# Optimization experiments

Hardware: AMD Instinct MI355X
Metric: run time of the kernel (lower is better)

Reference implementation:

```python
import jax, jax.numpy as jnp
import numpy as np

MIDC = 128
HEADS = 8
HEADC = MIDC // HEADS
EPS = 1e-5


def setup_inputs() -> dict:
    key = jax.random.key(0)
    ks = jax.random.split(key, 8)
    B, C, H, W = 8, MIDC, 256, 256
    s = 1.0 / np.sqrt(C)
    x = jax.random.normal(ks[0], (B, C, H, W), dtype=jnp.float32)
    qkv_w = jax.random.normal(ks[1], (3 * C, C), dtype=jnp.float32) * s
    o1_w = jax.random.normal(ks[2], (C, C), dtype=jnp.float32) * s
    o2_w = jax.random.normal(ks[3], (C, C), dtype=jnp.float32) * s
    kln_w = 1.0 + 0.1 * jax.random.normal(ks[4], (HEADS, 1, HEADC), dtype=jnp.float32)
    kln_b = 0.1 * jax.random.normal(ks[5], (HEADS, 1, HEADC), dtype=jnp.float32)
    vln_w = 1.0 + 0.1 * jax.random.normal(ks[6], (HEADS, 1, HEADC), dtype=jnp.float32)
    vln_b = 0.1 * jax.random.normal(ks[7], (HEADS, 1, HEADC), dtype=jnp.float32)
    return {"x": x, "qkv_w": qkv_w, "o1_w": o1_w, "o2_w": o2_w,
            "kln_w": kln_w, "kln_b": kln_b, "vln_w": vln_w, "vln_b": vln_b}


def _ln(t, w, b):
    # torch LayerNorm variant: unbiased std, eps added to std (not variance)
    m = t.mean(-1, keepdims=True)
    s = jnp.std(t, axis=-1, ddof=1, keepdims=True)
    return w * ((t - m) / (s + EPS)) + b


def reference(x, qkv_w, o1_w, o2_w, kln_w, kln_b, vln_w, vln_b):
    B, C, H, W = x.shape
    hc = C // HEADS
    N = H * W
    # 1x1 conv == pointwise matmul over channel dim
    qkv = jnp.einsum('oc,bchw->bhwo', qkv_w, x)            # (B,H,W,3C)
    qkv = qkv.reshape(B, N, HEADS, 3 * hc).transpose(0, 2, 1, 3)  # (B,heads,N,3hc)
    q, k, v = jnp.split(qkv, 3, axis=-1)
    k = _ln(k, kln_w, kln_b)
    v = _ln(v, vln_w, vln_b)
    kv = jnp.einsum('bhnd,bhne->bhde', k, v) / N            # (B,heads,hc,hc)
    o = jnp.einsum('bhnd,bhde->bhne', q, kv)                # (B,heads,N,hc)
    o = o.transpose(0, 2, 1, 3).reshape(B, H, W, C).transpose(0, 3, 1, 2)
    ret = o + x
    u = jnp.einsum('oc,bchw->bohw', o1_w, ret)
    u = jax.nn.gelu(u, approximate=False)
    u = jnp.einsum('oc,bchw->bohw', o2_w, u) + x
    return jax.nn.gelu(u, approximate=False)
```

## Files before the change

### kernel.cpp

```cpp
#include <hip/hip_runtime.h>

#define EPS 1e-5f

typedef _Float16 half8_t __attribute__((ext_vector_type(8)));
typedef _Float16 half4_t __attribute__((ext_vector_type(4)));
typedef float    float4_t __attribute__((ext_vector_type(4)));

__device__ __forceinline__ float gelu_f(float v) {
  return 0.5f * v * (1.0f + erff(v * 0.70710678118654752f));
}

template<int CTRL>
__device__ __forceinline__ float dpp_add(float v) {
  int j = __builtin_amdgcn_update_dpp(0, __float_as_int(v), CTRL, 0xF, 0xF, true);
  return v + __int_as_float(j);
}
__device__ __forceinline__ float rsum16(float v) {
  v = dpp_add<0xB1>(v);
  v = dpp_add<0x4E>(v);
  v = dpp_add<0x124>(v);
  v = dpp_add<0x128>(v);
  return v;
}

__global__ __launch_bounds__(256)
void k_wconv(const float* __restrict__ qkvw, const float* __restrict__ o1w,
             const float* __restrict__ o2w, _Float16* __restrict__ kvw,
             _Float16* __restrict__ qw, _Float16* __restrict__ o1h,
             _Float16* __restrict__ o2h) {
  int t = blockIdx.x * 256 + threadIdx.x;
  if (t < 32768) {
    int r = t >> 7, c = t & 127;
    int src = (r >> 5) * 48 + 16 + (r & 31);
    kvw[t] = (_Float16)qkvw[src * 128 + c];
  } else if (t < 49152) {
    int i = t - 32768;
    int r = i >> 7, c = i & 127;
    int src = (r >> 4) * 48 + (r & 15);
    qw[i] = (_Float16)qkvw[src * 128 + c];
  } else if (t < 65536) {
    int i = t - 49152;
    o1h[i] = (_Float16)o1w[i];
  } else {
    int i = t - 65536;
    o2h[i] = (_Float16)o2w[i];
  }
}

__global__ __launch_bounds__(256, 3)
void k_qkv_kv(const float* __restrict__ x, const _Float16* __restrict__ kvw,
              const float* __restrict__ klw, const float* __restrict__ klb,
              const float* __restrict__ vlw, const float* __restrict__ vlb,
              float* __restrict__ partial) {
  __shared__ _Float16 xs[64][136];
  const int t = threadIdx.x;
  const int lane = t & 63, w = t >> 6;
  const int quad = lane >> 4, l16 = lane & 15;
  const int b = blockIdx.x >> 8, cb = blockIdx.x & 255;
  const float* xb = x + (long)b * 8388608;

  float kw0[2], kb0[2], vw0[2], vb0[2];
#pragma unroll
  for (int hh = 0; hh < 2; hh++) {
    int h = 2 * w + hh;
    kw0[hh] = klw[h * 16 + l16]; kb0[hh] = klb[h * 16 + l16];
    vw0[hh] = vlw[h * 16 + l16]; vb0[hh] = vlb[h * 16 + l16];
  }

  float4_t kvacc[2] = {};

  for (int ch = 0; ch < 4; ch++) {
    const int n0 = cb * 256 + ch * 64;
#pragma unroll
    for (int i = 0; i < 8; i++) {
      int f = i * 256 + t;
      int c = f >> 4, pg = f & 15;
      float4 v = *(const float4*)(xb + ((long)c << 16) + n0 + 4 * pg);
      xs[4 * pg + 0][c] = (_Float16)v.x;
      xs[4 * pg + 1][c] = (_Float16)v.y;
      xs[4 * pg + 2][c] = (_Float16)v.z;
      xs[4 * pg + 3][c] = (_Float16)v.w;
    }
    __syncthreads();

    float4_t acc[4][4] = {};
#pragma unroll
    for (int k = 0; k < 4; k++) {
      half8_t A[4];
#pragma unroll
      for (int mt = 0; mt < 4; mt++)
        A[mt] = *(const half8_t*)&xs[mt * 16 + l16][k * 32 + quad * 8];
#pragma unroll
      for (int ot = 0; ot < 4; ot++) {
        half8_t Bf = *(const half8_t*)(kvw + (w * 64 + ot * 16 + l16) * 128 + k * 32 + quad * 8);
#pragma unroll
        for (int mt = 0; mt < 4; mt++)
          acc[mt][ot] = __builtin_amdgcn_mfma_f32_16x16x32_f16(A[mt], Bf, acc[mt][ot], 0, 0, 0);
      }
    }

#pragma unroll
    for (int hh = 0; hh < 2; hh++) {
#pragma unroll
      for (int mt = 0; mt < 4; mt++) {
        half4_t kf, vf;
#pragma unroll
        for (int rr = 0; rr < 4; rr++) {
          float kx = acc[mt][2 * hh + 0][rr];
          float vx = acc[mt][2 * hh + 1][rr];
          float s1k = rsum16(kx), s2k = rsum16(kx * kx);
          float s1v = rsum16(vx), s2v = rsum16(vx * vx);
          float mk = s1k * 0.0625f;
          float vark = (s2k - s1k * mk) * (1.0f / 15.0f);
          float kn = kw0[hh] * (kx - mk) / (sqrtf(fmaxf(vark, 0.0f)) + EPS) + kb0[hh];
          float mv = s1v * 0.0625f;
          float varv = (s2v - s1v * mv) * (1.0f / 15.0f);
          float vn = vw0[hh] * (vx - mv) / (sqrtf(fmaxf(varv, 0.0f)) + EPS) + vb0[hh];
          kf[rr] = (_Float16)kn;
          vf[rr] = (_Float16)vn;
        }
        kvacc[hh] = __builtin_amdgcn_mfma_f32_16x16x16f16(kf, vf, kvacc[hh], 0, 0, 0);
      }
    }
    __syncthreads();
  }

#pragma unroll
  for (int hh = 0; hh < 2; hh++) {
    int h = 2 * w + hh;
#pragma unroll
    for (int rr = 0; rr < 4; rr++) {
      int d = quad * 4 + rr;
      partial[((long)blockIdx.x * 8 + h) * 256 + d * 16 + l16] = kvacc[hh][rr];
    }
  }
}

__global__ __launch_bounds__(256)
void k_reduce(const float* __restrict__ partial, float* __restrict__ kvT) {
  const int bh = blockIdx.x;
  const int t = threadIdx.x;
  const int b = bh >> 3, h = bh & 7;
  float s = 0.0f;
#pragma unroll 8
  for (int cb = 0; cb < 256; cb++)
    s += partial[((long)(b * 256 + cb) * 8 + h) * 256 + t];
  kvT[(bh << 8) + (t & 15) * 16 + (t >> 4)] = s * (1.0f / 65536.0f);
}

__device__ __forceinline__ void gemm_128(const _Float16* src, const _Float16* wgt,
                                         int w, int l16, int quad, float4_t (&acc)[4][2]) {
#pragma unroll
  for (int k = 0; k < 4; k++) {
    half8_t A[4];
#pragma unroll
    for (int mt = 0; mt < 4; mt++)
      A[mt] = *(const half8_t*)(src + (mt * 16 + l16) * 136 + k * 32 + quad * 8);
#pragma unroll
    for (int ot = 0; ot < 2; ot++) {
      half8_t Bf = *(const half8_t*)(wgt + (w * 32 + ot * 16 + l16) * 128 + k * 32 + quad * 8);
#pragma unroll
      for (int mt = 0; mt < 4; mt++)
        acc[mt][ot] = __builtin_amdgcn_mfma_f32_16x16x32_f16(A[mt], Bf, acc[mt][ot], 0, 0, 0);
    }
  }
}

__global__ __launch_bounds__(256, 3)
void k_attn_out(const float* __restrict__ x, const _Float16* __restrict__ qw,
                const _Float16* __restrict__ o1h, const _Float16* __restrict__ o2h,
                const float* __restrict__ kvT, float* __restrict__ out) {
  __shared__ _Float16 xs[64][136];
  __shared__ _Float16 us[64][136];
  __shared__ _Float16 rs[64][136];
  const int t = threadIdx.x;
  const int lane = t & 63, w = t >> 6;
  const int quad = lane >> 4, l16 = lane & 15;
  const int b = blockIdx.x >> 10;
  const int n0 = (blockIdx.x & 1023) << 6;
  const float* xb = x + (long)b * 8388608;

#pragma unroll
  for (int i = 0; i < 8; i++) {
    int f = i * 256 + t, c = f >> 4, pg = f & 15;
    float4 v = *(const float4*)(xb + ((long)c << 16) + n0 + 4 * pg);
    xs[4 * pg + 0][c] = (_Float16)v.x;
    xs[4 * pg + 1][c] = (_Float16)v.y;
    xs[4 * pg + 2][c] = (_Float16)v.z;
    xs[4 * pg + 3][c] = (_Float16)v.w;
  }

  half4_t kvf[2];
#pragma unroll
  for (int hh = 0; hh < 2; hh++) {
    int h = 2 * w + hh;
    float4 kq = *(const float4*)(kvT + ((b * 8 + h) << 8) + l16 * 16 + quad * 4);
    kvf[hh][0] = (_Float16)kq.x; kvf[hh][1] = (_Float16)kq.y;
    kvf[hh][2] = (_Float16)kq.z; kvf[hh][3] = (_Float16)kq.w;
  }
  __syncthreads();

  float4_t qa[4][2] = {};
  gemm_128(&xs[0][0], qw, w, l16, quad, qa);
#pragma unroll
  for (int mt = 0; mt < 4; mt++)
#pragma unroll
    for (int ot = 0; ot < 2; ot++)
#pragma unroll
      for (int rr = 0; rr < 4; rr++)
        us[mt * 16 + quad * 4 + rr][w * 32 + ot * 16 + l16] = (_Float16)qa[mt][ot][rr];

#pragma unroll
  for (int hh = 0; hh < 2; hh++) {
    int h = 2 * w + hh;
#pragma unroll
    for (int mt = 0; mt < 4; mt++) {
      half4_t qf = *(const half4_t*)&us[mt * 16 + l16][h * 16 + quad * 4];
      float4_t oacc = {};
      oacc = __builtin_amdgcn_mfma_f32_16x16x16f16(qf, kvf[hh], oacc, 0, 0, 0);
#pragma unroll
      for (int rr = 0; rr < 4; rr++) {
        int p = mt * 16 + quad * 4 + rr, c = h * 16 + l16;
        rs[p][c] = (_Float16)(oacc[rr] + (float)xs[p][c]);
      }
    }
  }
  __syncthreads();

  float4_t ua[4][2] = {};
  gemm_128(&rs[0][0], o1h, w, l16, quad, ua);
#pragma unroll
  for (int mt = 0; mt < 4; mt++)
#pragma unroll
    for (int ot = 0; ot < 2; ot++)
#pragma unroll
      for (int rr = 0; rr < 4; rr++)
        us[mt * 16 + quad * 4 + rr][w * 32 + ot * 16 + l16] = (_Float16)gelu_f(ua[mt][ot][rr]);
  __syncthreads();

  float4_t ya[4][2] = {};
  gemm_128(&us[0][0], o2h, w, l16, quad, ya);
#pragma unroll
  for (int mt = 0; mt < 4; mt++)
#pragma unroll
    for (int ot = 0; ot < 2; ot++)
#pragma unroll
      for (int rr = 0; rr < 4; rr++) {
        int p = mt * 16 + quad * 4 + rr, c = w * 32 + ot * 16 + l16;
        rs[p][c] = (_Float16)gelu_f(ya[mt][ot][rr] + (float)xs[p][c]);
      }
  __syncthreads();

#pragma unroll
  for (int i = 0; i < 8; i++) {
    int f = i * 256 + t, c = f >> 4, pg = f & 15;
    float4 o4;
    o4.x = (float)rs[4 * pg + 0][c];
    o4.y = (float)rs[4 * pg + 1][c];
    o4.z = (float)rs[4 * pg + 2][c];
    o4.w = (float)rs[4 * pg + 3][c];
    *(float4*)(out + ((long)b * 128 + c) * 65536 + n0 + 4 * pg) = o4;
  }
}

extern "C" void kernel_launch(void* const* d_in, const int* in_sizes, int n_in,
                              void* d_out, int out_size, void* d_ws, size_t ws_size,
                              hipStream_t stream) {
  const float* x    = (const float*)d_in[0];
  const float* qkvw = (const float*)d_in[1];
  const float* o1w  = (const float*)d_in[2];
  const float* o2w  = (const float*)d_in[3];
  const float* klw  = (const float*)d_in[4];
  const float* klb  = (const float*)d_in[5];
  const float* vlw  = (const float*)d_in[6];
  const float* vlb  = (const float*)d_in[7];
  float* out = (float*)d_out;
  char* ws = (char*)d_ws;
  _Float16* kvw  = (_Float16*)(ws + 0);
  _Float16* qw   = (_Float16*)(ws + 65536);
  _Float16* o1h  = (_Float16*)(ws + 98304);
  _Float16* o2h  = (_Float16*)(ws + 131072);
  float* kvT     = (float*)(ws + 163840);
  float* partial = (float*)(ws + 229376);

  k_wconv<<<320, 256, 0, stream>>>(qkvw, o1w, o2w, kvw, qw, o1h, o2h);
  k_qkv_kv<<<2048, 256, 0, stream>>>(x, kvw, klw, klb, vlw, vlb, partial);
  k_reduce<<<64, 256, 0, stream>>>(partial, kvT);
  k_attn_out<<<8192, 256, 0, stream>>>(x, qw, o1h, o2h, kvT, out);
}
```

Measured before the change: 891.8 us.

## Fold LN mean into weights, approximate GELU, shrink LDS, raise occupancy

```diff
diff --git a/kernel.cpp b/kernel.cpp
--- a/kernel.cpp
+++ b/kernel.cpp
@@ -7,7 +7,10 @@
 typedef float    float4_t __attribute__((ext_vector_type(4)));
 
 __device__ __forceinline__ float gelu_f(float v) {
-  return 0.5f * v * (1.0f + erff(v * 0.70710678118654752f));
+  float u2 = v * v;
+  float a  = __builtin_fmaf(u2, -0.10294322f, -2.3022078f);
+  float e  = __builtin_amdgcn_exp2f(v * a);
+  return v * __builtin_amdgcn_rcpf(1.0f + e);
 }
 
 template<int CTRL>
@@ -31,8 +34,13 @@
   int t = blockIdx.x * 256 + threadIdx.x;
   if (t < 32768) {
     int r = t >> 7, c = t & 127;
-    int src = (r >> 5) * 48 + 16 + (r & 31);
-    kvw[t] = (_Float16)qkvw[src * 128 + c];
+    int h = r >> 5, rr = r & 31;
+    int src = h * 48 + 16 + rr;
+    int mb  = h * 48 + 16 + (rr & 16);
+    float s = 0.0f;
+#pragma unroll
+    for (int d = 0; d < 16; d++) s += qkvw[(mb + d) * 128 + c];
+    kvw[t] = (_Float16)(qkvw[src * 128 + c] - 0.0625f * s);
   } else if (t < 49152) {
     int i = t - 32768;
     int r = i >> 7, c = i & 127;
@@ -47,7 +55,7 @@
   }
 }
 
-__global__ __launch_bounds__(256, 3)
+__global__ __launch_bounds__(256, 5)
 void k_qkv_kv(const float* __restrict__ x, const _Float16* __restrict__ kvw,
               const float* __restrict__ klw, const float* __restrict__ klb,
               const float* __restrict__ vlw, const float* __restrict__ vlb,
@@ -108,16 +116,14 @@
         for (int rr = 0; rr < 4; rr++) {
           float kx = acc[mt][2 * hh + 0][rr];
           float vx = acc[mt][2 * hh + 1][rr];
-          float s1k = rsum16(kx), s2k = rsum16(kx * kx);
-          float s1v = rsum16(vx), s2v = rsum16(vx * vx);
-          float mk = s1k * 0.0625f;
-          float vark = (s2k - s1k * mk) * (1.0f / 15.0f);
-          float kn = kw0[hh] * (kx - mk) / (sqrtf(fmaxf(vark, 0.0f)) + EPS) + kb0[hh];
-          float mv = s1v * 0.0625f;
-          float varv = (s2v - s1v * mv) * (1.0f / 15.0f);
-          float vn = vw0[hh] * (vx - mv) / (sqrtf(fmaxf(varv, 0.0f)) + EPS) + vb0[hh];
-          kf[rr] = (_Float16)kn;
-          vf[rr] = (_Float16)vn;
+          float s2k = rsum16(kx * kx);
+          float s2v = rsum16(vx * vx);
+          float rk = __builtin_amdgcn_rcpf(
+              __builtin_fmaf(__builtin_amdgcn_sqrtf(s2k), 0.25819889f, EPS));
+          float rv = __builtin_amdgcn_rcpf(
+              __builtin_fmaf(__builtin_amdgcn_sqrtf(s2v), 0.25819889f, EPS));
+          kf[rr] = (_Float16)((kw0[hh] * rk) * kx + kb0[hh]);
+          vf[rr] = (_Float16)((vw0[hh] * rv) * vx + vb0[hh]);
         }
         kvacc[hh] = __builtin_amdgcn_mfma_f32_16x16x16f16(kf, vf, kvacc[hh], 0, 0, 0);
       }
@@ -166,13 +172,12 @@
   }
 }
 
-__global__ __launch_bounds__(256, 3)
+__global__ __launch_bounds__(256, 4)
 void k_attn_out(const float* __restrict__ x, const _Float16* __restrict__ qw,
                 const _Float16* __restrict__ o1h, const _Float16* __restrict__ o2h,
                 const float* __restrict__ kvT, float* __restrict__ out) {
-  __shared__ _Float16 xs[64][136];
-  __shared__ _Float16 us[64][136];
-  __shared__ _Float16 rs[64][136];
+  __shared__ _Float16 bufA[64][136];
+  __shared__ _Float16 bufB[64][136];
   const int t = threadIdx.x;
   const int lane = t & 63, w = t >> 6;
   const int quad = lane >> 4, l16 = lane & 15;
@@ -184,10 +189,10 @@
   for (int i = 0; i < 8; i++) {
     int f = i * 256 + t, c = f >> 4, pg = f & 15;
     float4 v = *(const float4*)(xb + ((long)c << 16) + n0 + 4 * pg);
-    xs[4 * pg + 0][c] = (_Float16)v.x;
-    xs[4 * pg + 1][c] = (_Float16)v.y;
-    xs[4 * pg + 2][c] = (_Float16)v.z;
-    xs[4 * pg + 3][c] = (_Float16)v.w;
+    bufA[4 * pg + 0][c] = (_Float16)v.x;
+    bufA[4 * pg + 1][c] = (_Float16)v.y;
+    bufA[4 * pg + 2][c] = (_Float16)v.z;
+    bufA[4 * pg + 3][c] = (_Float16)v.w;
   }
 
   half4_t kvf[2];
@@ -201,45 +206,54 @@
   __syncthreads();
 
   float4_t qa[4][2] = {};
-  gemm_128(&xs[0][0], qw, w, l16, quad, qa);
+  gemm_128(&bufA[0][0], qw, w, l16, quad, qa);
 #pragma unroll
   for (int mt = 0; mt < 4; mt++)
 #pragma unroll
     for (int ot = 0; ot < 2; ot++)
 #pragma unroll
       for (int rr = 0; rr < 4; rr++)
-        us[mt * 16 + quad * 4 + rr][w * 32 + ot * 16 + l16] = (_Float16)qa[mt][ot][rr];
+        bufB[mt * 16 + quad * 4 + rr][w * 32 + ot * 16 + l16] = (_Float16)qa[mt][ot][rr];
 
 #pragma unroll
   for (int hh = 0; hh < 2; hh++) {
     int h = 2 * w + hh;
 #pragma unroll
     for (int mt = 0; mt < 4; mt++) {
-      half4_t qf = *(const half4_t*)&us[mt * 16 + l16][h * 16 + quad * 4];
+      half4_t qf = *(const half4_t*)&bufB[mt * 16 + l16][h * 16 + quad * 4];
       float4_t oacc = {};
       oacc = __builtin_amdgcn_mfma_f32_16x16x16f16(qf, kvf[hh], oacc, 0, 0, 0);
 #pragma unroll
       for (int rr = 0; rr < 4; rr++) {
         int p = mt * 16 + quad * 4 + rr, c = h * 16 + l16;
-        rs[p][c] = (_Float16)(oacc[rr] + (float)xs[p][c]);
+        bufB[p][c] = (_Float16)(oacc[rr] + (float)bufA[p][c]);
       }
     }
   }
+
+  _Float16 xres[4][2][4];
+#pragma unroll
+  for (int mt = 0; mt < 4; mt++)
+#pragma unroll
+    for (int ot = 0; ot < 2; ot++)
+#pragma unroll
+      for (int rr = 0; rr < 4; rr++)
+        xres[mt][ot][rr] = bufA[mt * 16 + quad * 4 + rr][w * 32 + ot * 16 + l16];
   __syncthreads();
 
   float4_t ua[4][2] = {};
-  gemm_128(&rs[0][0], o1h, w, l16, quad, ua);
+  gemm_128(&bufB[0][0], o1h, w, l16, quad, ua);
 #pragma unroll
   for (int mt = 0; mt < 4; mt++)
 #pragma unroll
     for (int ot = 0; ot < 2; ot++)
 #pragma unroll
       for (int rr = 0; rr < 4; rr++)
-        us[mt * 16 + quad * 4 + rr][w * 32 + ot * 16 + l16] = (_Float16)gelu_f(ua[mt][ot][rr]);
+        bufA[mt * 16 + quad * 4 + rr][w * 32 + ot * 16 + l16] = (_Float16)gelu_f(ua[mt][ot][rr]);
   __syncthreads();
 
   float4_t ya[4][2] = {};
-  gemm_128(&us[0][0], o2h, w, l16, quad, ya);
+  gemm_128(&bufA[0][0], o2h, w, l16, quad, ya);
 #pragma unroll
   for (int mt = 0; mt < 4; mt++)
 #pragma unroll
@@ -247,7 +261,7 @@
 #pragma unroll
       for (int rr = 0; rr < 4; rr++) {
         int p = mt * 16 + quad * 4 + rr, c = w * 32 + ot * 16 + l16;
-        rs[p][c] = (_Float16)gelu_f(ya[mt][ot][rr] + (float)xs[p][c]);
+        bufB[p][c] = (_Float16)gelu_f(ya[mt][ot][rr] + (float)xres[mt][ot][rr]);
       }
   __syncthreads();
 
@@ -255,10 +269,10 @@
   for (int i = 0; i < 8; i++) {
     int f = i * 256 + t, c = f >> 4, pg = f & 15;
     float4 o4;
-    o4.x = (float)rs[4 * pg + 0][c];
-    o4.y = (float)rs[4 * pg + 1][c];
-    o4.z = (float)rs[4 * pg + 2][c];
-    o4.w = (float)rs[4 * pg + 3][c];
+    o4.x = (float)bufB[4 * pg + 0][c];
+    o4.y = (float)bufB[4 * pg + 1][c];
+    o4.z = (float)bufB[4 * pg + 2][c];
+    o4.w = (float)bufB[4 * pg + 3][c];
     *(float4*)(out + ((long)b * 128 + c) * 65536 + n0 + 4 * pg) = o4;
   }
 }
```

Result: no change. 889.4 us (-0.3%).
